# Performance work log

Measured on AMD Instinct MI355X. Metric: run time of the kernel, lower is better.

The kernel has to match this reference:

```python
import jax, jax.numpy as jnp
import numpy as np

HSPACES = [1024, 1024, 1024, 1024]   # hypothesis-space sizes
C = 3                                 # num_of_classifiers
EPSILON = 10                          # max rejection-sampling attempts
BATCH = 8192
# tensor_split at cumulative boundaries -> item counts per policy split
ITEM_COUNTS = [HSPACES[0] + HSPACES[1]] + list(HSPACES[2:])  # [2048, 1024, 1024]
HALL = sum(HSPACES)  # 4096


def setup_inputs() -> dict:
    key = jax.random.key(0)
    kx, kw, kb = jax.random.split(key, 3)
    X = jax.random.normal(kx, (BATCH, HALL * C), dtype=jnp.float32)
    W = jax.random.normal(kw, (len(ITEM_COUNTS), C), dtype=jnp.float32) * 0.1
    b = jax.random.normal(kb, (len(ITEM_COUNTS),), dtype=jnp.float32) * 0.1
    return {"X": X, "W": W, "b": b}


def _scores(X, W, b):
    # per-split Linear(3,1) + softmax over items, then concat -> (B, HALL)
    parts = []
    start = 0
    for d, n in enumerate(ITEM_COUNTS):
        obs = X[:, start:start + n * C].reshape(-1, n, C)          # (B, n, 3)
        logits = jnp.einsum('bnc,c->bn', obs, W[d]) + b[d]          # (B, n)
        parts.append(jax.nn.softmax(logits, axis=1))
        start += n * C
    return jnp.concatenate(parts, axis=1)                           # (B, HALL)


def reference(X, W, b):
    scores = _scores(X, W, b)                                       # (B, HALL) probs
    logp = jnp.log(scores)
    key = jax.random.key(42)
    B = scores.shape[0]
    # vectorized epsilon rejection sampling: draw EPSILON samples per row;
    # take `best` if any draw hits it (loop breaks there), else the last draw
    samples = jax.random.categorical(key, logp, shape=(EPSILON, B))  # (EPS, B)
    best = jnp.argmax(scores, axis=1)                                # (B,)
    hit = (samples == best[None, :]).any(axis=0)                     # (B,)
    actions = jnp.where(hit, best, samples[-1])
    return actions
```

## Files before the change

### kernel.cpp

```cpp
#include <hip/hip_runtime.h>
#include <stdint.h>

#define BATCH   8192
#define HALL    4096
#define TPB     256
#define PERT    (HALL / TPB)
#define EPS     10
#define BH      33554432u

__device__ __forceinline__ uint32_t rotl32(uint32_t x, int r) {
    return (x << r) | (x >> (32 - r));
}

__device__ __forceinline__ uint32_t threefry_bits_k42(uint32_t lo) {
    const uint32_t ks0 = 0u;
    const uint32_t ks1 = 42u;
    const uint32_t ks2 = 0x1BD11BDAu ^ 42u;
    uint32_t x0 = 0u + ks0;
    uint32_t x1 = lo + ks1;
#define TF_R(r) { x0 += x1; x1 = rotl32(x1, r); x1 ^= x0; }
    TF_R(13) TF_R(15) TF_R(26) TF_R(6)   x0 += ks1; x1 += ks2 + 1u;
    TF_R(17) TF_R(29) TF_R(16) TF_R(24)  x0 += ks2; x1 += ks0 + 2u;
    TF_R(13) TF_R(15) TF_R(26) TF_R(6)   x0 += ks0; x1 += ks1 + 3u;
    TF_R(17) TF_R(29) TF_R(16) TF_R(24)  x0 += ks1; x1 += ks2 + 4u;
    TF_R(13) TF_R(15) TF_R(26) TF_R(6)   x0 += ks2; x1 += ks0 + 5u;
#undef TF_R
    return x0 ^ x1;
}

__device__ __forceinline__ float gumbel_exact(uint32_t bits) {
    const float tiny = 1.1754943508222875e-38f;
    uint32_t fb = (bits >> 9) | 0x3F800000u;
    float f = __uint_as_float(fb) - 1.0f;
    float u = fmaxf(tiny, f * 1.0f + tiny);
    float a = -logf(u);
    return -logf(a);
}

__device__ __forceinline__ float block_max(float v, float* swf, int tid) {
    for (int off = 32; off; off >>= 1)
        v = fmaxf(v, __shfl_down(v, off, 64));
    if ((tid & 63) == 0) swf[tid >> 6] = v;
    __syncthreads();
    float r = fmaxf(fmaxf(swf[0], swf[1]), fmaxf(swf[2], swf[3]));
    __syncthreads();
    return r;
}

__device__ __forceinline__ float block_sum(float v, float* swf, int tid) {
    for (int off = 32; off; off >>= 1)
        v += __shfl_down(v, off, 64);
    if ((tid & 63) == 0) swf[tid >> 6] = v;
    __syncthreads();
    float r = ((swf[0] + swf[1]) + swf[2]) + swf[3];
    __syncthreads();
    return r;
}

__device__ __forceinline__ void block_argmax(float v, int i, float* swf, int* swi,
                                             int tid, float& rv, int& ri) {
    for (int off = 32; off; off >>= 1) {
        float ov = __shfl_down(v, off, 64);
        int   oi = __shfl_down(i, off, 64);
        if (ov > v || (ov == v && oi < i)) { v = ov; i = oi; }
    }
    if ((tid & 63) == 0) { swf[tid >> 6] = v; swi[tid >> 6] = i; }
    __syncthreads();
    rv = swf[0]; ri = swi[0];
#pragma unroll
    for (int w = 1; w < 4; w++) {
        float ov = swf[w]; int oi = swi[w];
        if (ov > rv || (ov == rv && oi < ri)) { rv = ov; ri = oi; }
    }
    __syncthreads();
}

__global__ __launch_bounds__(TPB)
void reinforce_kernel(const float* __restrict__ X, const float* __restrict__ W,
                      const float* __restrict__ bias, int* __restrict__ out) {
#pragma clang fp contract(off)
    __shared__ float s_logp[HALL];
    __shared__ float swf[4];
    __shared__ int   swi[4];

    const int b   = blockIdx.x;
    const int tid = threadIdx.x;
    const float* xr = X + (size_t)b * (HALL * 3);

    const float w00 = W[0], w01 = W[1], w02 = W[2], bb0 = bias[0];
    const float w10 = W[3], w11 = W[4], w12 = W[5], bb1 = bias[1];
    const float w20 = W[6], w21 = W[7], w22 = W[8], bb2 = bias[2];

    float lg[PERT];
#pragma unroll
    for (int j = 0; j < PERT; j++) {
        int h = tid + j * TPB;
        float x0 = xr[3 * h], x1 = xr[3 * h + 1], x2 = xr[3 * h + 2];
        float wa, wb, wc, bb;
        if (j < 8)       { wa = w00; wb = w01; wc = w02; bb = bb0; }
        else if (j < 12) { wa = w10; wb = w11; wc = w12; bb = bb1; }
        else             { wa = w20; wb = w21; wc = w22; bb = bb2; }
        lg[j] = ((x0 * wa + x1 * wb) + x2 * wc) + bb;
    }

    float pm0 = -INFINITY, pm1 = -INFINITY, pm2 = -INFINITY;
#pragma unroll
    for (int j = 0; j < PERT; j++) {
        if (j < 8)       pm0 = fmaxf(pm0, lg[j]);
        else if (j < 12) pm1 = fmaxf(pm1, lg[j]);
        else             pm2 = fmaxf(pm2, lg[j]);
    }
    float m0 = block_max(pm0, swf, tid);
    float m1 = block_max(pm1, swf, tid);
    float m2 = block_max(pm2, swf, tid);

    float ex[PERT];
    float ps0 = 0.f, ps1 = 0.f, ps2 = 0.f;
#pragma unroll
    for (int j = 0; j < PERT; j++) {
        float m = (j < 8) ? m0 : (j < 12) ? m1 : m2;
        float e = expf(lg[j] - m);
        ex[j] = e;
        if (j < 8)       ps0 += e;
        else if (j < 12) ps1 += e;
        else             ps2 += e;
    }
    float s0 = block_sum(ps0, swf, tid);
    float s1 = block_sum(ps1, swf, tid);
    float s2 = block_sum(ps2, swf, tid);

    float bv = -INFINITY; int bi = 0;
#pragma unroll
    for (int j = 0; j < PERT; j++) {
        float s = (j < 8) ? s0 : (j < 12) ? s1 : s2;
        float p = ex[j] / s;
        int h = tid + j * TPB;
        if (p > bv) { bv = p; bi = h; }
        s_logp[h] = logf(p);
    }
    __syncthreads();

    float rbv; int best;
    block_argmax(bv, bi, swf, swi, tid, rbv, best);

    float sv[EPS]; int si[EPS];
#pragma unroll
    for (int e = 0; e < EPS; e++) { sv[e] = -INFINITY; si[e] = 0x7fffffff; }

    const uint32_t rowbase = (uint32_t)b * (uint32_t)HALL;
    for (int j = 0; j < PERT; j++) {
        int h = tid + j * TPB;
        float lp = s_logp[h];
        uint32_t cnt = rowbase + (uint32_t)h;
#pragma unroll
        for (int e = 0; e < EPS; e++) {
            uint32_t bits = threefry_bits_k42(cnt + (uint32_t)e * BH);
            float v = gumbel_exact(bits) + lp;
            if (v > sv[e]) { sv[e] = v; si[e] = h; }
        }
    }

    int samp[EPS];
#pragma unroll
    for (int e = 0; e < EPS; e++) {
        float rv; int ri;
        block_argmax(sv[e], si[e], swf, swi, tid, rv, ri);
        samp[e] = ri;
    }

    if (tid == 0) {
        bool hit = false;
#pragma unroll
        for (int e = 0; e < EPS; e++) hit = hit || (samp[e] == best);
        out[b] = hit ? best : samp[EPS - 1];
    }
}

extern "C" void kernel_launch(void* const* d_in, const int* in_sizes, int n_in,
                              void* d_out, int out_size, void* d_ws, size_t ws_size,
                              hipStream_t stream) {
    const float* X    = (const float*)d_in[0];
    const float* W    = (const float*)d_in[1];
    const float* bias = (const float*)d_in[2];
    int* out = (int*)d_out;
    (void)in_sizes; (void)n_in; (void)d_ws; (void)ws_size; (void)out_size;

    reinforce_kernel<<<BATCH, TPB, 0, stream>>>(X, W, bias, out);
}
```

Measured before the change: 1.219 ms.

## Replace Gumbel argmax with p/(-log u) ratio comparison and batch block reductions

The Gumbel-max selection argmax(-log(-log u) + log p) is rewritten as argmax p / (-log u), compared by cross-multiplication. This removes one logf per draw and the per-element logf(p). The separate max, sum and argmax block reductions are merged so that all three splits and all eleven argmax reductions share a single barrier each, which removes many __syncthreads. The change risks mismatched samples versus the reference when values are nearly tied, because the reordered floating-point comparisons can round differently and the epsilon offset on u is replaced by a plain clamp.

```diff
diff --git a/kernel.cpp b/kernel.cpp
--- a/kernel.cpp
+++ b/kernel.cpp
@@ -4,7 +4,7 @@
 #define BATCH   8192
 #define HALL    4096
 #define TPB     256
-#define PERT    (HALL / TPB)
+#define PERT    16
 #define EPS     10
 #define BH      33554432u
 
@@ -28,63 +28,20 @@
     return x0 ^ x1;
 }
 
-__device__ __forceinline__ float gumbel_exact(uint32_t bits) {
-    const float tiny = 1.1754943508222875e-38f;
-    uint32_t fb = (bits >> 9) | 0x3F800000u;
-    float f = __uint_as_float(fb) - 1.0f;
-    float u = fmaxf(tiny, f * 1.0f + tiny);
-    float a = -logf(u);
-    return -logf(a);
-}
-
-__device__ __forceinline__ float block_max(float v, float* swf, int tid) {
-    for (int off = 32; off; off >>= 1)
-        v = fmaxf(v, __shfl_down(v, off, 64));
-    if ((tid & 63) == 0) swf[tid >> 6] = v;
-    __syncthreads();
-    float r = fmaxf(fmaxf(swf[0], swf[1]), fmaxf(swf[2], swf[3]));
-    __syncthreads();
-    return r;
-}
-
-__device__ __forceinline__ float block_sum(float v, float* swf, int tid) {
-    for (int off = 32; off; off >>= 1)
-        v += __shfl_down(v, off, 64);
-    if ((tid & 63) == 0) swf[tid >> 6] = v;
-    __syncthreads();
-    float r = ((swf[0] + swf[1]) + swf[2]) + swf[3];
-    __syncthreads();
-    return r;
-}
-
-__device__ __forceinline__ void block_argmax(float v, int i, float* swf, int* swi,
-                                             int tid, float& rv, int& ri) {
-    for (int off = 32; off; off >>= 1) {
-        float ov = __shfl_down(v, off, 64);
-        int   oi = __shfl_down(i, off, 64);
-        if (ov > v || (ov == v && oi < i)) { v = ov; i = oi; }
-    }
-    if ((tid & 63) == 0) { swf[tid >> 6] = v; swi[tid >> 6] = i; }
-    __syncthreads();
-    rv = swf[0]; ri = swi[0];
-#pragma unroll
-    for (int w = 1; w < 4; w++) {
-        float ov = swf[w]; int oi = swi[w];
-        if (ov > rv || (ov == rv && oi < ri)) { rv = ov; ri = oi; }
-    }
-    __syncthreads();
-}
-
 __global__ __launch_bounds__(TPB)
 void reinforce_kernel(const float* __restrict__ X, const float* __restrict__ W,
                       const float* __restrict__ bias, int* __restrict__ out) {
 #pragma clang fp contract(off)
-    __shared__ float s_logp[HALL];
-    __shared__ float swf[4];
-    __shared__ int   swi[4];
+    __shared__ float s_p[HALL];
+    __shared__ float s_rm[3][4];
+    __shared__ float s_rs[3][4];
+    __shared__ float s_rv[EPS + 1][4];
+    __shared__ int   s_ri[EPS + 1][4];
 
     const int b   = blockIdx.x;
     const int tid = threadIdx.x;
+    const int wv  = tid >> 6;
+    const int ln  = tid & 63;
     const float* xr = X + (size_t)b * (HALL * 3);
 
     const float w00 = W[0], w01 = W[1], w02 = W[2], bb0 = bias[0];
@@ -110,9 +67,16 @@
         else if (j < 12) pm1 = fmaxf(pm1, lg[j]);
         else             pm2 = fmaxf(pm2, lg[j]);
     }
-    float m0 = block_max(pm0, swf, tid);
-    float m1 = block_max(pm1, swf, tid);
-    float m2 = block_max(pm2, swf, tid);
+    for (int off = 32; off; off >>= 1) {
+        pm0 = fmaxf(pm0, __shfl_down(pm0, off, 64));
+        pm1 = fmaxf(pm1, __shfl_down(pm1, off, 64));
+        pm2 = fmaxf(pm2, __shfl_down(pm2, off, 64));
+    }
+    if (ln == 0) { s_rm[0][wv] = pm0; s_rm[1][wv] = pm1; s_rm[2][wv] = pm2; }
+    __syncthreads();
+    const float m0 = fmaxf(fmaxf(s_rm[0][0], s_rm[0][1]), fmaxf(s_rm[0][2], s_rm[0][3]));
+    const float m1 = fmaxf(fmaxf(s_rm[1][0], s_rm[1][1]), fmaxf(s_rm[1][2], s_rm[1][3]));
+    const float m2 = fmaxf(fmaxf(s_rm[2][0], s_rm[2][1]), fmaxf(s_rm[2][2], s_rm[2][3]));
 
     float ex[PERT];
     float ps0 = 0.f, ps1 = 0.f, ps2 = 0.f;
@@ -125,9 +89,16 @@
         else if (j < 12) ps1 += e;
         else             ps2 += e;
     }
-    float s0 = block_sum(ps0, swf, tid);
-    float s1 = block_sum(ps1, swf, tid);
-    float s2 = block_sum(ps2, swf, tid);
+    for (int off = 32; off; off >>= 1) {
+        ps0 += __shfl_down(ps0, off, 64);
+        ps1 += __shfl_down(ps1, off, 64);
+        ps2 += __shfl_down(ps2, off, 64);
+    }
+    if (ln == 0) { s_rs[0][wv] = ps0; s_rs[1][wv] = ps1; s_rs[2][wv] = ps2; }
+    __syncthreads();
+    const float s0 = ((s_rs[0][0] + s_rs[0][1]) + s_rs[0][2]) + s_rs[0][3];
+    const float s1 = ((s_rs[1][0] + s_rs[1][1]) + s_rs[1][2]) + s_rs[1][3];
+    const float s2 = ((s_rs[2][0] + s_rs[2][1]) + s_rs[2][2]) + s_rs[2][3];
 
     float bv = -INFINITY; int bi = 0;
 #pragma unroll
@@ -136,43 +107,72 @@
         float p = ex[j] / s;
         int h = tid + j * TPB;
         if (p > bv) { bv = p; bi = h; }
-        s_logp[h] = logf(p);
+        s_p[h] = p;
     }
-    __syncthreads();
 
-    float rbv; int best;
-    block_argmax(bv, bi, swf, swi, tid, rbv, best);
-
-    float sv[EPS]; int si[EPS];
+    const float tiny = 1.1754943508222875e-38f;
+    float apv[EPS]; float aav[EPS]; int aix[EPS];
 #pragma unroll
-    for (int e = 0; e < EPS; e++) { sv[e] = -INFINITY; si[e] = 0x7fffffff; }
+    for (int e = 0; e < EPS; e++) { apv[e] = 0.0f; aav[e] = 1.0f; aix[e] = 0x7fffffff; }
 
     const uint32_t rowbase = (uint32_t)b * (uint32_t)HALL;
+#pragma unroll 1
     for (int j = 0; j < PERT; j++) {
         int h = tid + j * TPB;
-        float lp = s_logp[h];
+        float pj = s_p[h];
         uint32_t cnt = rowbase + (uint32_t)h;
 #pragma unroll
         for (int e = 0; e < EPS; e++) {
             uint32_t bits = threefry_bits_k42(cnt + (uint32_t)e * BH);
-            float v = gumbel_exact(bits) + lp;
-            if (v > sv[e]) { sv[e] = v; si[e] = h; }
+            uint32_t fb = (bits >> 9) | 0x3F800000u;
+            float f = __uint_as_float(fb) - 1.0f;
+            float u = fmaxf(f, tiny);
+            float a = -logf(u);
+            if (pj * aav[e] > apv[e] * a) { apv[e] = pj; aav[e] = a; aix[e] = h; }
         }
     }
 
-    int samp[EPS];
 #pragma unroll
     for (int e = 0; e < EPS; e++) {
-        float rv; int ri;
-        block_argmax(sv[e], si[e], swf, swi, tid, rv, ri);
-        samp[e] = ri;
+        float r = apv[e] / aav[e];
+        int   i = aix[e];
+        for (int off = 32; off; off >>= 1) {
+            float rv = __shfl_down(r, off, 64);
+            int   ri = __shfl_down(i, off, 64);
+            if (rv > r || (rv == r && ri < i)) { r = rv; i = ri; }
+        }
+        if (ln == 0) { s_rv[e][wv] = r; s_ri[e][wv] = i; }
     }
+    {
+        float r = bv; int i = bi;
+        for (int off = 32; off; off >>= 1) {
+            float rv = __shfl_down(r, off, 64);
+            int   ri = __shfl_down(i, off, 64);
+            if (rv > r || (rv == r && ri < i)) { r = rv; i = ri; }
+        }
+        if (ln == 0) { s_rv[EPS][wv] = r; s_ri[EPS][wv] = i; }
+    }
+    __syncthreads();
 
     if (tid == 0) {
-        bool hit = false;
+        int samp[EPS];
 #pragma unroll
-        for (int e = 0; e < EPS; e++) hit = hit || (samp[e] == best);
-        out[b] = hit ? best : samp[EPS - 1];
+        for (int e = 0; e <= EPS; e++) {
+            float r = s_rv[e][0]; int i = s_ri[e][0];
+#pragma unroll
+            for (int w = 1; w < 4; w++) {
+                float rv = s_rv[e][w]; int ri = s_ri[e][w];
+                if (rv > r || (rv == r && ri < i)) { r = rv; i = ri; }
+            }
+            if (e < EPS) samp[e] = i;
+            else {
+                int best = i;
+                bool hit = false;
+#pragma unroll
+                for (int k = 0; k < EPS; k++) hit = hit || (samp[k] == best);
+                out[b] = hit ? best : samp[EPS - 1];
+            }
+        }
     }
 }
 
```

Measured after the change: 1.132 ms. -7.1%, faster.
